# Kernel tuning notes

Measured on AMD Instinct MI355X. Metric: run time of the kernel, lower is better.

## Reference

```python
import jax, jax.numpy as jnp
import numpy as np

DIM = 512
N_HEADS = 8
HEAD_DIM = DIM // N_HEADS
BN_EPS = 1e-5


def setup_inputs() -> dict:
    key = jax.random.key(0)
    ks = jax.random.split(key, 8)
    B, C, H, W = 16, DIM, 32, 32
    x = jax.random.normal(ks[0], (B, C, H, W), dtype=jnp.float32)
    # 1x1 convs == channel matmuls: stacked q/k/v weights [3, out, in], proj [out, in]
    w_qkv = jax.random.normal(ks[1], (3, DIM, DIM), dtype=jnp.float32) * (DIM ** -0.5)
    w_proj = jax.random.normal(ks[2], (DIM, DIM), dtype=jnp.float32) * (DIM ** -0.5)
    # BatchNorm (inference form) params for q/k/v branches, stacked [3, C]
    bn_gamma = jax.random.uniform(ks[3], (3, DIM), minval=0.5, maxval=1.5)
    bn_beta = jax.random.normal(ks[4], (3, DIM)) * 0.1
    bn_mean = jax.random.normal(ks[5], (3, DIM)) * 0.1
    bn_var = jax.random.uniform(ks[6], (3, DIM), minval=0.5, maxval=1.5)
    return {"x": x, "w_qkv": w_qkv, "w_proj": w_proj, "bn_gamma": bn_gamma,
            "bn_beta": bn_beta, "bn_mean": bn_mean, "bn_var": bn_var}


def _ternary_ste(t):
    # forward: sign(t) in {-1,0,1}; backward: identity (straight-through)
    return t + jax.lax.stop_gradient(jnp.sign(t) - t)


def reference(x, w_qkv, w_proj, bn_gamma, bn_beta, bn_mean, bn_var):
    B, C, H, W = x.shape
    N = H * W
    xf = x.reshape(B, C, N)
    # fused 1x1 conv for q,k,v: [3,B,C,N]
    qkv = jnp.einsum('koc,bcn->kbon', w_qkv, xf)
    # BatchNorm (inference): y = (x - mean)/sqrt(var+eps)*gamma + beta
    s = bn_gamma / jnp.sqrt(bn_var + BN_EPS)          # [3,C]
    b = bn_beta - bn_mean * s                          # [3,C]
    qkv = qkv * s[:, None, :, None] + b[:, None, :, None]
    q = _ternary_ste(qkv[0]).reshape(B, N_HEADS, HEAD_DIM, N)
    k = _ternary_ste(qkv[1]).reshape(B, N_HEADS, HEAD_DIM, N)
    v = qkv[2].reshape(B, N_HEADS, HEAD_DIM, N)
    scale = HEAD_DIM ** -0.5
    attn = jnp.einsum('bhdn,bhen->bhde', q, k) * scale  # [B,h,d,d] channel-wise attn
    attn = jax.nn.softmax(attn, axis=-1)
    out = jnp.einsum('bhde,bhen->bhdn', attn, v).reshape(B, C, N)
    out = jnp.einsum('oc,bcn->bon', w_proj, out) + xf   # proj + residual
    return out.reshape(B, C, H, W)
```

## Files before the change

kernel.cpp:

```cpp
#include <hip/hip_runtime.h>
#include <math.h>

#define BN_EPS 1e-5f
#define FIXC 1.0e-4f

typedef _Float16 f16;
typedef _Float16 f16x4 __attribute__((ext_vector_type(4)));
typedef _Float16 f16x8 __attribute__((ext_vector_type(8)));
typedef float f32x4 __attribute__((ext_vector_type(4)));
typedef int i32x4 __attribute__((ext_vector_type(4)));

static constexpr int BB = 16;
static constexpr int C  = 512;
static constexpr int NP = 1024;
static constexpr int NH = 8;
static constexpr int HD = 64;
static constexpr int M3 = 1536;


static constexpr size_t OFF_WHI  = 0;
static constexpr size_t OFF_WLO  = 1572864;
static constexpr size_t OFF_WPH  = 3145728;
static constexpr size_t OFF_SB   = 3670016;
static constexpr size_t OFF_WN   = 3682304;
static constexpr size_t OFF_XN   = 3686400;
static constexpr size_t OFF_FLAG = 3751936;
static constexpr size_t OFF_XTH  = 5849088;
static constexpr size_t OFF_XTL  = 22626304;
static constexpr size_t OFF_AOT  = OFF_XTH;
static constexpr size_t OFF_Q    = 39403520;
static constexpr size_t OFF_K    = 47792128;
static constexpr size_t OFF_VT   = 56180736;

__device__ __forceinline__ void gld16(const void* g, void* l) {
  __builtin_amdgcn_global_load_lds(
      (const __attribute__((address_space(1))) void*)g,
      (__attribute__((address_space(3))) void*)l, 16, 0, 0);
}

__device__ __forceinline__ size_t frag_off(int tile, int kt, int row7, int k5) {
  return (((size_t)tile * 16 + kt) * 8 + (row7 >> 4)) * 512
       + (size_t)((row7 & 15) | ((k5 >> 3) << 4)) * 8;
}

__global__ __launch_bounds__(256) void k_convW(
    const float* __restrict__ wqkv, const float* __restrict__ wproj,
    const float* __restrict__ g, const float* __restrict__ be,
    const float* __restrict__ mu, const float* __restrict__ va,
    f16* __restrict__ Whi, f16* __restrict__ Wlo, f16* __restrict__ Wph,
    float* __restrict__ sA, float* __restrict__ bA, float* __restrict__ wnorm)
{
  const int i = blockIdx.x * 256 + threadIdx.x;
  {
    const int m = i >> 6, l = i & 63;
    const float4 v0 = *(const float4*)&wqkv[(size_t)m * C + l * 8];
    const float4 v1 = *(const float4*)&wqkv[(size_t)m * C + l * 8 + 4];
    const float vv[8] = {v0.x, v0.y, v0.z, v0.w, v1.x, v1.y, v1.z, v1.w};
    f16x8 hv, lv;
    float s2 = 0.f;
#pragma unroll
    for (int q = 0; q < 8; ++q) {
      const f16 h = (f16)vv[q];
      hv[q] = h; lv[q] = (f16)(vv[q] - (float)h);
      s2 = fmaf(vv[q], vv[q], s2);
    }
    *(f16x8*)&Whi[frag_off(m >> 7, l >> 2, m & 127, (l & 3) * 8)] = hv;
    *(f16x8*)&Wlo[(size_t)m * C + l * 8] = lv;
    if (m < 1024) {
      s2 += __shfl_xor(s2, 1);  s2 += __shfl_xor(s2, 2);
      s2 += __shfl_xor(s2, 4);  s2 += __shfl_xor(s2, 8);
      s2 += __shfl_xor(s2, 16); s2 += __shfl_xor(s2, 32);
      if (l == 0) wnorm[m] = sqrtf(s2);
    }
  }
  if (i < 32768) {
    const int m = i >> 6, l = i & 63;
    const float4 v0 = *(const float4*)&wproj[(size_t)m * C + l * 8];
    const float4 v1 = *(const float4*)&wproj[(size_t)m * C + l * 8 + 4];
    const float vv[8] = {v0.x, v0.y, v0.z, v0.w, v1.x, v1.y, v1.z, v1.w};
    f16x8 hv;
#pragma unroll
    for (int q = 0; q < 8; ++q) hv[q] = (f16)vv[q];
    *(f16x8*)&Wph[frag_off(m >> 7, l >> 2, m & 127, (l & 3) * 8)] = hv;
  }
  if (i < M3) {
    const float s = g[i] / sqrtf(va[i] + BN_EPS);
    sA[i] = s;
    bA[i] = be[i] - mu[i] * s;
  }
}

__global__ __launch_bounds__(256) void k_convX(
    const float* __restrict__ x, f16* __restrict__ XtH, f16* __restrict__ XtL,
    float* __restrict__ xnorm2)
{
  const int k0 = blockIdx.x * 64, n0 = blockIdx.y * 64, b = blockIdx.z;
  __shared__ float ls[64][65];
  const int t = threadIdx.x;
  const float* xp = x + ((size_t)b * C + k0) * NP + n0;
  const int c4 = (t & 15) * 4, r0 = t >> 4;
#pragma unroll
  for (int q = 0; q < 4; ++q) {
    const float4 v = *(const float4*)(xp + (size_t)(r0 + q * 16) * NP + c4);
    ls[r0 + q * 16][c4 + 0] = v.x; ls[r0 + q * 16][c4 + 1] = v.y;
    ls[r0 + q * 16][c4 + 2] = v.z; ls[r0 + q * 16][c4 + 3] = v.w;
  }
  __syncthreads();
  if (t < 64) {
    float s2 = 0.f;
#pragma unroll
    for (int q = 0; q < 64; ++q) { const float v = ls[q][t]; s2 = fmaf(v, v, s2); }
    atomicAdd(&xnorm2[(b << 10) + n0 + t], s2);
  }
  const int n = t >> 2, kk = (t & 3) * 16;
  const int n_abs = n0 + n;
  f16x8 hv0 = {}, hv1 = {}, lv0 = {}, lv1 = {};
#pragma unroll
  for (int q = 0; q < 8; ++q) {
    const float v = ls[kk + q][n];
    const f16 h = (f16)v;
    hv0[q] = h; lv0[q] = (f16)(v - (float)h);
  }
#pragma unroll
  for (int q = 0; q < 8; ++q) {
    const float v = ls[kk + 8 + q][n];
    const f16 h = (f16)v;
    hv1[q] = h; lv1[q] = (f16)(v - (float)h);
  }
  const int kb0 = k0 + kk, kb1 = k0 + kk + 8;
  *(f16x8*)&XtH[frag_off(b * 8 + (n_abs >> 7), kb0 >> 5, n_abs & 127, kb0 & 31)] = hv0;
  *(f16x8*)&XtH[frag_off(b * 8 + (n_abs >> 7), kb1 >> 5, n_abs & 127, kb1 & 31)] = hv1;
  *(f16x8*)&XtL[((size_t)b * NP + n_abs) * C + kb0] = lv0;
  *(f16x8*)&XtL[((size_t)b * NP + n_abs) * C + kb1] = lv1;
}

__global__ __launch_bounds__(64, 3) void k_qkv_mfma(
    const f16* __restrict__ Whi, const f16* __restrict__ XtH,
    const float* __restrict__ sA, const float* __restrict__ bA,
    const float* __restrict__ wnorm, const float* __restrict__ xnorm2,
    signed char* __restrict__ qw, signed char* __restrict__ kw,
    f16* __restrict__ vt, unsigned* __restrict__ flagbits)
{
  __shared__ __align__(16) f16 SMEM[64 * 72];

  const int lane = threadIdx.x;
  const int n0 = blockIdx.x * 64, m0 = blockIdx.y * 64, b = blockIdx.z;

  const f16* Af = Whi + (size_t)(m0 >> 7) * 65536;
  const f16* Bf = XtH + ((size_t)b * 8 + (n0 >> 7)) * 65536;
  const int ab = (m0 >> 4) & 7;
  const int bb = (n0 >> 4) & 7;

  f32x4 acc[4][4];
#pragma unroll
  for (int i = 0; i < 4; ++i)
#pragma unroll
    for (int j = 0; j < 4; ++j) acc[i][j] = (f32x4){0.f, 0.f, 0.f, 0.f};

  const int lr = lane & 15, ls = lane >> 4;

#define LOADF(KT, AR, BR) do {                                          \
    _Pragma("unroll")                                                   \
    for (int i_ = 0; i_ < 4; ++i_) {                                    \
      (AR)[i_] = *(const f16x8*)&Af[((size_t)(KT) * 8 + ab + i_) * 512 + lane * 8]; \
      (BR)[i_] = *(const f16x8*)&Bf[((size_t)(KT) * 8 + bb + i_) * 512 + lane * 8]; \
    }                                                                   \
  } while (0)

#define COMPF(AR, BR) do {                                              \
    _Pragma("unroll")                                                   \
    for (int i_ = 0; i_ < 4; ++i_)                                      \
      _Pragma("unroll")                                                 \
      for (int j_ = 0; j_ < 4; ++j_)                                    \
        acc[i_][j_] = __builtin_amdgcn_mfma_f32_16x16x32_f16(           \
            (AR)[i_], (BR)[j_], acc[i_][j_], 0, 0, 0);                  \
  } while (0)

  {
    f16x8 a0[4], b0[4], a1[4], b1[4];
    LOADF(0, a0, b0);
#pragma unroll
    for (int kt = 0; kt < 16; kt += 2) {
      LOADF(kt + 1, a1, b1);
      COMPF(a0, b0);
      if (kt + 2 < 16) LOADF(kt + 2, a0, b0);
      COMPF(a1, b1);
    }
  }

#undef LOADF
#undef COMPF

  const int kidx = m0 >> 9;
  if (kidx != 2) {
    signed char* dst0 = (kidx == 0) ? qw : kw;
    float xnrm[4];
#pragma unroll
    for (int j = 0; j < 4; ++j)
      xnrm[j] = sqrtf(xnorm2[(b << 10) + n0 + j * 16 + lr]);
#pragma unroll
    for (int i = 0; i < 4; ++i) {
      float sv[4], bv[4], dl[4];
#pragma unroll
      for (int r = 0; r < 4; ++r) {
        const int o = m0 + i * 16 + ls * 4 + r;
        sv[r] = sA[o]; bv[r] = bA[o];
        dl[r] = FIXC * wnorm[o] * sv[r];
      }
      const int oc0 = (m0 & 511) + i * 16 + ls * 4;
      const int og0 = m0 + i * 16 + ls * 4;
#pragma unroll
      for (int j = 0; j < 4; ++j) {
        const int n = n0 + j * 16 + lr;
#pragma unroll
        for (int r = 0; r < 4; ++r) {
          const float z = fmaf(acc[i][j][r], sv[r], bv[r]);
          dst0[((size_t)b * C + oc0 + r) * NP + n] =
              (signed char)((z > 0.f) - (z < 0.f));
          if (fabsf(z) <= dl[r] * xnrm[j]) {
            const int of = og0 + r;
            atomicOr(&flagbits[(((size_t)b * NP + n) << 5) + (of >> 5)],
                     1u << (of & 31));
          }
        }
      }
    }
  } else {
    const int c0 = m0 & 511;
#pragma unroll
    for (int i = 0; i < 4; ++i) {
      float sv[4], bv[4];
#pragma unroll
      for (int r = 0; r < 4; ++r) {
        const int o = m0 + i * 16 + ls * 4 + r;
        sv[r] = sA[o]; bv[r] = bA[o];
      }
#pragma unroll
      for (int j = 0; j < 4; ++j) {
        f16x4 pk;
#pragma unroll
        for (int r = 0; r < 4; ++r)
          pk[r] = (f16)fmaf(acc[i][j][r], sv[r], bv[r]);
        *(f16x4*)&SMEM[(size_t)(j * 16 + lr) * 72 + i * 16 + ls * 4] = pk;
      }
    }
    __syncthreads();
    f16* dstv = vt + ((size_t)b * NP + n0 + lane) * C + c0;
#pragma unroll
    for (int q = 0; q < 8; ++q) {
      const f16x8 rq = *(const f16x8*)&SMEM[(size_t)lane * 72 + q * 8];
      *(f16x8*)(dstv + q * 8) = rq;
    }
  }
}

__global__ __launch_bounds__(256) void k_fix(
    const unsigned* __restrict__ flagbits,
    const f16* __restrict__ Whi, const f16* __restrict__ Wlo,
    const f16* __restrict__ XtH, const f16* __restrict__ XtL,
    const float* __restrict__ sA, const float* __restrict__ bA,
    signed char* __restrict__ qw, signed char* __restrict__ kw)
{
  const int wv = blockIdx.x * 4 + (threadIdx.x >> 6);
  const int lane = threadIdx.x & 63;
  const int b = wv >> 10, n = wv & 1023;

  const unsigned* bm = flagbits + ((size_t)wv << 5);
  const unsigned myw = (lane < 32) ? bm[lane] : 0u;
  if (__ballot(myw != 0) == 0ULL) return;

  const int kb = lane * 8;
  const f16x8 bhv = *(const f16x8*)&XtH[
      frag_off(b * 8 + (n >> 7), kb >> 5, n & 127, kb & 31)];
  const f16x8 blv = *(const f16x8*)&XtL[((size_t)b * NP + n) * C + kb];
  float xv[8];
#pragma unroll
  for (int q = 0; q < 8; ++q) xv[q] = (float)bhv[q] + (float)blv[q];

  for (int w = 0; w < 32; ++w) {
    unsigned bits = __shfl(myw, w);
    while (bits) {
      const int o = w * 32 + __builtin_ctz(bits);
      bits &= bits - 1;
      const f16x8 ahv = *(const f16x8*)&Whi[
          frag_off(o >> 7, kb >> 5, o & 127, kb & 31)];
      const f16x8 alv = *(const f16x8*)&Wlo[(size_t)o * C + kb];
      float s = 0.f;
#pragma unroll
      for (int q = 0; q < 8; ++q)
        s = fmaf((float)ahv[q] + (float)alv[q], xv[q], s);
      s += __shfl_xor(s, 1);  s += __shfl_xor(s, 2);  s += __shfl_xor(s, 4);
      s += __shfl_xor(s, 8);  s += __shfl_xor(s, 16); s += __shfl_xor(s, 32);
      if (lane == 0) {
        const float y = fmaf(s, sA[o], bA[o]);
        const signed char sg = (signed char)((y > 0.f) - (y < 0.f));
        if (o < 512) qw[((size_t)b * C + o) * NP + n] = sg;
        else         kw[((size_t)b * C + (o - 512)) * NP + n] = sg;
      }
    }
  }
}

__global__ __launch_bounds__(256) void k_attn_fused(
    const signed char* __restrict__ qw, const signed char* __restrict__ kw,
    const f16* __restrict__ vt, f16* __restrict__ aot)
{
  const int half = blockIdx.x;
  const int bh = blockIdx.y;
  const int b = bh >> 3, h = bh & 7;
  const int t = threadIdx.x, lane = t & 63, wid = t >> 6;
  const int dw = wid * 16;
  const int lr = lane & 15, lg = lane >> 4;

  __shared__ f16 ph[64][72];
  __shared__ f16 pl[64][72];
  __shared__ f16 sb[64][72];

  const signed char* qp = qw + ((size_t)b * C + h * HD + dw + lr) * NP;
  const signed char* kp = kw + ((size_t)b * C + h * HD + lr) * NP;

  i32x4 accS[4];
#pragma unroll
  for (int j = 0; j < 4; ++j) accS[j] = (i32x4){0, 0, 0, 0};

#pragma unroll 4
  for (int ks = 0; ks < 16; ++ks) {
    const i32x4 af = *(const i32x4*)(qp + ks * 64 + lg * 16);
#pragma unroll
    for (int j = 0; j < 4; ++j) {
      const i32x4 bf = *(const i32x4*)(kp + (size_t)(j * 16) * NP + ks * 64 + lg * 16);
      accS[j] = __builtin_amdgcn_mfma_i32_16x16x64_i8(af, bf, accS[j], 0, 0, 0);
    }
  }

#pragma unroll
  for (int r = 0; r < 4; ++r) {
    float mx = (float)accS[0][r];
#pragma unroll
    for (int j = 1; j < 4; ++j) mx = fmaxf(mx, (float)accS[j][r]);
    mx = fmaxf(mx, __shfl_xor(mx, 1));
    mx = fmaxf(mx, __shfl_xor(mx, 2));
    mx = fmaxf(mx, __shfl_xor(mx, 4));
    mx = fmaxf(mx, __shfl_xor(mx, 8));
    float pvv[4];
    float sm = 0.f;
#pragma unroll
    for (int j = 0; j < 4; ++j) {
      pvv[j] = expf(((float)accS[j][r] - mx) * 0.125f);
      sm += pvv[j];
    }
    sm += __shfl_xor(sm, 1);
    sm += __shfl_xor(sm, 2);
    sm += __shfl_xor(sm, 4);
    sm += __shfl_xor(sm, 8);
    const float inv = 1.f / sm;
    const int drow = dw + lg * 4 + r;
#pragma unroll
    for (int j = 0; j < 4; ++j) {
      const float p = pvv[j] * inv;
      const f16 hi = (f16)p;
      ph[drow][j * 16 + lr] = hi;
      pl[drow][j * 16 + lr] = (f16)(p - (float)hi);
    }
  }
  __syncthreads();

  const f16x8 pa0h = *(const f16x8*)&ph[dw + lr][lg * 8];
  const f16x8 pa0l = *(const f16x8*)&pl[dw + lr][lg * 8];
  const f16x8 pa1h = *(const f16x8*)&ph[dw + lr][32 + lg * 8];
  const f16x8 pa1l = *(const f16x8*)&pl[dw + lr][32 + lg * 8];

  const f16* vbase = vt + (size_t)b * NP * C + h * HD;
  const int nbase = half * 512;

  for (int nc = 0; nc < 8; ++nc) {
    const int nn0 = nbase + nc * 64;
    __syncthreads();
#pragma unroll
    for (int nt = 0; nt < 4; ++nt) {
      const f16* vp = vbase + (size_t)(nn0 + nt * 16 + lr) * C + lg * 8;
      const f16x8 bv0 = *(const f16x8*)(vp);
      const f16x8 bv1 = *(const f16x8*)(vp + 32);
      f32x4 acc = (f32x4){0.f, 0.f, 0.f, 0.f};
      acc = __builtin_amdgcn_mfma_f32_16x16x32_f16(pa0h, bv0, acc, 0, 0, 0);
      acc = __builtin_amdgcn_mfma_f32_16x16x32_f16(pa0l, bv0, acc, 0, 0, 0);
      acc = __builtin_amdgcn_mfma_f32_16x16x32_f16(pa1h, bv1, acc, 0, 0, 0);
      acc = __builtin_amdgcn_mfma_f32_16x16x32_f16(pa1l, bv1, acc, 0, 0, 0);
      f16x4 pk;
#pragma unroll
      for (int r = 0; r < 4; ++r) pk[r] = (f16)acc[r];
      *(f16x4*)&sb[nt * 16 + lr][dw + lg * 4] = pk;
    }
    __syncthreads();
    const int nl = t >> 2, cc = (t & 3) * 16;
    const f16x8 o0 = *(const f16x8*)&sb[nl][cc];
    const f16x8 o1 = *(const f16x8*)&sb[nl][cc + 8];
    const int n_abs = nn0 + nl;
    const int c1 = h * HD + cc, c2 = h * HD + cc + 8;
    *(f16x8*)&aot[frag_off(b * 8 + (n_abs >> 7), c1 >> 5, n_abs & 127, c1 & 31)] = o0;
    *(f16x8*)&aot[frag_off(b * 8 + (n_abs >> 7), c2 >> 5, n_abs & 127, c2 & 31)] = o1;
  }
}

__global__ __launch_bounds__(256) void k_proj_mfma(
    const f16* __restrict__ Wph, const f16* __restrict__ aot,
    const float* __restrict__ X, float* __restrict__ out)
{
  __shared__ __align__(16) f16 SMEM[32768];
  f16* const As0 = SMEM;
  f16* const Bs0 = SMEM + 8192;
  f16* const As1 = SMEM + 16384;
  f16* const Bs1 = SMEM + 24576;

  const int t = threadIdx.x, lane = t & 63, wid = t >> 6;
  const int n0 = blockIdx.x * 128, m0 = blockIdx.y * 128, b = blockIdx.z;

  const f16* Af = Wph + (size_t)(m0 >> 7) * 65536;
  const f16* Bf = aot + ((size_t)b * 8 + (n0 >> 7)) * 65536;

  f32x4 acc[4][4];
#pragma unroll
  for (int i = 0; i < 4; ++i)
#pragma unroll
    for (int j = 0; j < 4; ++j) acc[i][j] = (f32x4){0.f, 0.f, 0.f, 0.f};

  const int wm = wid >> 1, wn = wid & 1;
  const int lr = lane & 15, ls = lane >> 4;
  const int soff = wid * 512 + lane * 8;

#define PSTAGE(TI, AS, BS) do {                                         \
    const f16* Ak_ = Af + (size_t)(TI) * 8192;                          \
    const f16* Bk_ = Bf + (size_t)(TI) * 8192;                          \
    _Pragma("unroll")                                                   \
    for (int r_ = 0; r_ < 4; ++r_) {                                    \
      gld16(Ak_ + r_ * 2048 + soff, &(AS)[r_ * 2048 + wid * 512]);      \
      gld16(Bk_ + r_ * 2048 + soff, &(BS)[r_ * 2048 + wid * 512]);      \
    }                                                                   \
  } while (0)

#define PCOMP(AS, BS) do {                                              \
    _Pragma("unroll")                                                   \
    for (int ksub_ = 0; ksub_ < 2; ++ksub_) {                           \
      f16x8 ah_[4], bh_[4];                                             \
      _Pragma("unroll")                                                 \
      for (int i_ = 0; i_ < 4; ++i_) {                                  \
        ah_[i_] = *(const f16x8*)&(AS)[ksub_ * 4096 + (wm * 4 + i_) * 512 + lane * 8]; \
        bh_[i_] = *(const f16x8*)&(BS)[ksub_ * 4096 + (wn * 4 + i_) * 512 + lane * 8]; \
      }                                                                 \
      _Pragma("unroll")                                                 \
      for (int i_ = 0; i_ < 4; ++i_)                                    \
        _Pragma("unroll")                                               \
        for (int j_ = 0; j_ < 4; ++j_)                                  \
          acc[i_][j_] = __builtin_amdgcn_mfma_f32_16x16x32_f16(         \
              ah_[i_], bh_[j_], acc[i_][j_], 0, 0, 0);                  \
    }                                                                   \
  } while (0)

  PSTAGE(0, As0, Bs0);
#pragma unroll
  for (int ti = 0; ti < 8; ++ti) {
    if (ti < 7) {
      if (ti & 1) PSTAGE(ti + 1, As0, Bs0);
      else        PSTAGE(ti + 1, As1, Bs1);
      asm volatile("s_waitcnt vmcnt(8)" ::: "memory");
    } else {
      asm volatile("s_waitcnt vmcnt(0)" ::: "memory");
    }
    __builtin_amdgcn_sched_barrier(0);
    __builtin_amdgcn_s_barrier();
    if (ti & 1) PCOMP(As1, Bs1); else PCOMP(As0, Bs0);
    asm volatile("s_waitcnt lgkmcnt(0)" ::: "memory");
    __builtin_amdgcn_sched_barrier(0);
    __builtin_amdgcn_s_barrier();
  }

#undef PSTAGE
#undef PCOMP

#pragma unroll
  for (int i = 0; i < 4; ++i) {
    const int oc0 = m0 + wm * 64 + i * 16 + ls * 4;
#pragma unroll
    for (int j = 0; j < 4; ++j) {
      const int n = n0 + wn * 64 + j * 16 + lr;
#pragma unroll
      for (int r = 0; r < 4; ++r) {
        const size_t idx = ((size_t)b * C + oc0 + r) * NP + n;
        out[idx] = acc[i][j][r] + X[idx];
      }
    }
  }
}

extern "C" void kernel_launch(void* const* d_in, const int* in_sizes, int n_in,
                              void* d_out, int out_size, void* d_ws, size_t ws_size,
                              hipStream_t stream)
{
  const float* x      = (const float*)d_in[0];
  const float* w_qkv  = (const float*)d_in[1];
  const float* w_proj = (const float*)d_in[2];
  const float* g      = (const float*)d_in[3];
  const float* be     = (const float*)d_in[4];
  const float* mu     = (const float*)d_in[5];
  const float* va     = (const float*)d_in[6];
  float* out = (float*)d_out;

  char* ws = (char*)d_ws;
  f16*  Whi = (f16*)(ws + OFF_WHI);
  f16*  Wlo = (f16*)(ws + OFF_WLO);
  f16*  Wph = (f16*)(ws + OFF_WPH);
  float* sA = (float*)(ws + OFF_SB);
  float* bA = sA + M3;
  float* wn = (float*)(ws + OFF_WN);
  float* xn2 = (float*)(ws + OFF_XN);
  unsigned* flagbits = (unsigned*)(ws + OFF_FLAG);
  f16*  XtH = (f16*)(ws + OFF_XTH);
  f16*  XtL = (f16*)(ws + OFF_XTL);
  f16*  aot = (f16*)(ws + OFF_AOT);
  signed char* qw = (signed char*)(ws + OFF_Q);
  signed char* kw = (signed char*)(ws + OFF_K);
  f16*  vtw = (f16*)(ws + OFF_VT);

  hipMemsetAsync(xn2, 0, OFF_XTH - OFF_XN, stream);

  k_convW<<<dim3(384), 256, 0, stream>>>(
      w_qkv, w_proj, g, be, mu, va, Whi, Wlo, Wph, sA, bA, wn);
  k_convX<<<dim3(C / 64, NP / 64, BB), 256, 0, stream>>>(x, XtH, XtL, xn2);
  k_qkv_mfma<<<dim3(NP / 64, M3 / 64, BB), 64, 0, stream>>>(
      Whi, XtH, sA, bA, wn, xn2, qw, kw, vtw, flagbits);
  k_fix<<<dim3(BB * NP / 4), 256, 0, stream>>>(
      flagbits, Whi, Wlo, XtH, XtL, sA, bA, qw, kw);
  k_attn_fused<<<dim3(2, BB * NH), 256, 0, stream>>>(qw, kw, vtw, aot);
  k_proj_mfma<<<dim3(NP / 128, C / 128, BB), 256, 0, stream>>>(Wph, aot, x, out);
}
```

Baseline: 145.8 us.

## Retile QKV GEMM to 256x256 block tiles with double-buffered LDS staging

```diff
diff --git a/kernel.cpp b/kernel.cpp
--- a/kernel.cpp
+++ b/kernel.cpp
@@ -134,62 +134,82 @@
   *(f16x8*)&XtL[((size_t)b * NP + n_abs) * C + kb1] = lv1;
 }
 
-__global__ __launch_bounds__(64, 3) void k_qkv_mfma(
+__global__ __launch_bounds__(512, 1) void k_qkv_mfma(
     const f16* __restrict__ Whi, const f16* __restrict__ XtH,
     const float* __restrict__ sA, const float* __restrict__ bA,
     const float* __restrict__ wnorm, const float* __restrict__ xnorm2,
     signed char* __restrict__ qw, signed char* __restrict__ kw,
     f16* __restrict__ vt, unsigned* __restrict__ flagbits)
 {
-  __shared__ __align__(16) f16 SMEM[64 * 72];
-
-  const int lane = threadIdx.x;
-  const int n0 = blockIdx.x * 64, m0 = blockIdx.y * 64, b = blockIdx.z;
+  __shared__ __align__(16) f16 SMEM[65536];
+  f16* const As0 = SMEM;
+  f16* const Bs0 = SMEM + 16384;
+  f16* const As1 = SMEM + 32768;
+  f16* const Bs1 = SMEM + 49152;
+
+  const int t = threadIdx.x, lane = t & 63, wid = t >> 6;
+  const int n0 = blockIdx.x * 256, m0 = blockIdx.y * 256, b = blockIdx.z;
 
   const f16* Af = Whi + (size_t)(m0 >> 7) * 65536;
   const f16* Bf = XtH + ((size_t)b * 8 + (n0 >> 7)) * 65536;
-  const int ab = (m0 >> 4) & 7;
-  const int bb = (n0 >> 4) & 7;
-
-  f32x4 acc[4][4];
-#pragma unroll
-  for (int i = 0; i < 4; ++i)
+
+  f32x4 acc[8][4];
+#pragma unroll
+  for (int i = 0; i < 8; ++i)
 #pragma unroll
     for (int j = 0; j < 4; ++j) acc[i][j] = (f32x4){0.f, 0.f, 0.f, 0.f};
 
+  const int wm = wid >> 2, wn = wid & 3;
   const int lr = lane & 15, ls = lane >> 4;
 
-#define LOADF(KT, AR, BR) do {                                          \
+#define QSTAGE(S, AS, BS) do {                                          \
     _Pragma("unroll")                                                   \
-    for (int i_ = 0; i_ < 4; ++i_) {                                    \
-      (AR)[i_] = *(const f16x8*)&Af[((size_t)(KT) * 8 + ab + i_) * 512 + lane * 8]; \
-      (BR)[i_] = *(const f16x8*)&Bf[((size_t)(KT) * 8 + bb + i_) * 512 + lane * 8]; \
+    for (int u_ = 0; u_ < 4; ++u_) {                                    \
+      const size_t so_ = (size_t)(u_ >> 1) * 65536 +                    \
+                         (size_t)(2 * (S) + (u_ & 1)) * 4096 + t * 8;   \
+      gld16(Af + so_, &(AS)[u_ * 4096 + wid * 512]);                    \
+      gld16(Bf + so_, &(BS)[u_ * 4096 + wid * 512]);                    \
     }                                                                   \
   } while (0)
 
-#define COMPF(AR, BR) do {                                              \
-    _Pragma("unroll")                                                   \
-    for (int i_ = 0; i_ < 4; ++i_)                                      \
-      _Pragma("unroll")                                                 \
-      for (int j_ = 0; j_ < 4; ++j_)                                    \
-        acc[i_][j_] = __builtin_amdgcn_mfma_f32_16x16x32_f16(           \
-            (AR)[i_], (BR)[j_], acc[i_][j_], 0, 0, 0);                  \
-  } while (0)
-
-  {
-    f16x8 a0[4], b0[4], a1[4], b1[4];
-    LOADF(0, a0, b0);
-#pragma unroll
-    for (int kt = 0; kt < 16; kt += 2) {
-      LOADF(kt + 1, a1, b1);
-      COMPF(a0, b0);
-      if (kt + 2 < 16) LOADF(kt + 2, a0, b0);
-      COMPF(a1, b1);
-    }
-  }
-
-#undef LOADF
-#undef COMPF
+  QSTAGE(0, As0, Bs0);
+#pragma unroll
+  for (int s = 0; s < 8; ++s) {
+    if (s < 7) {
+      if (s & 1) QSTAGE(s + 1, As0, Bs0);
+      else       QSTAGE(s + 1, As1, Bs1);
+      asm volatile("s_waitcnt vmcnt(8)" ::: "memory");
+    } else {
+      asm volatile("s_waitcnt vmcnt(0)" ::: "memory");
+    }
+    __builtin_amdgcn_sched_barrier(0);
+    __builtin_amdgcn_s_barrier();
+    const f16* AS = (s & 1) ? As1 : As0;
+    const f16* BS = (s & 1) ? Bs1 : Bs0;
+#pragma unroll
+    for (int ph = 0; ph < 4; ++ph) {
+      const int mh = ph & 1, ksub = ph >> 1;
+      f16x8 ah[4], bh[4];
+#pragma unroll
+      for (int ii = 0; ii < 4; ++ii)
+        ah[ii] = *(const f16x8*)&AS[((wm * 2 + ksub) * 8 + mh * 4 + ii) * 512 + lane * 8];
+#pragma unroll
+      for (int j = 0; j < 4; ++j)
+        bh[j] = *(const f16x8*)&BS[(((wn >> 1) * 2 + ksub) * 8 + (wn & 1) * 4 + j) * 512 + lane * 8];
+      __builtin_amdgcn_s_setprio(1);
+#pragma unroll
+      for (int ii = 0; ii < 4; ++ii)
+#pragma unroll
+        for (int j = 0; j < 4; ++j)
+          acc[mh * 4 + ii][j] = __builtin_amdgcn_mfma_f32_16x16x32_f16(
+              ah[ii], bh[j], acc[mh * 4 + ii][j], 0, 0, 0);
+      __builtin_amdgcn_s_setprio(0);
+    }
+    asm volatile("s_waitcnt lgkmcnt(0)" ::: "memory");
+    __builtin_amdgcn_sched_barrier(0);
+    __builtin_amdgcn_s_barrier();
+  }
+#undef QSTAGE
 
   const int kidx = m0 >> 9;
   if (kidx != 2) {
@@ -197,21 +217,21 @@
     float xnrm[4];
 #pragma unroll
     for (int j = 0; j < 4; ++j)
-      xnrm[j] = sqrtf(xnorm2[(b << 10) + n0 + j * 16 + lr]);
-#pragma unroll
-    for (int i = 0; i < 4; ++i) {
+      xnrm[j] = sqrtf(xnorm2[(b << 10) + n0 + wn * 64 + j * 16 + lr]);
+#pragma unroll
+    for (int i = 0; i < 8; ++i) {
       float sv[4], bv[4], dl[4];
 #pragma unroll
       for (int r = 0; r < 4; ++r) {
-        const int o = m0 + i * 16 + ls * 4 + r;
+        const int o = m0 + wm * 128 + i * 16 + ls * 4 + r;
         sv[r] = sA[o]; bv[r] = bA[o];
         dl[r] = FIXC * wnorm[o] * sv[r];
       }
-      const int oc0 = (m0 & 511) + i * 16 + ls * 4;
-      const int og0 = m0 + i * 16 + ls * 4;
+      const int oc0 = (m0 & 511) + wm * 128 + i * 16 + ls * 4;
+      const int og0 = m0 + wm * 128 + i * 16 + ls * 4;
 #pragma unroll
       for (int j = 0; j < 4; ++j) {
-        const int n = n0 + j * 16 + lr;
+        const int n = n0 + wn * 64 + j * 16 + lr;
 #pragma unroll
         for (int r = 0; r < 4; ++r) {
           const float z = fmaf(acc[i][j][r], sv[r], bv[r]);
@@ -227,29 +247,35 @@
     }
   } else {
     const int c0 = m0 & 511;
-#pragma unroll
-    for (int i = 0; i < 4; ++i) {
-      float sv[4], bv[4];
-#pragma unroll
-      for (int r = 0; r < 4; ++r) {
-        const int o = m0 + i * 16 + ls * 4 + r;
-        sv[r] = sA[o]; bv[r] = bA[o];
+    for (int hc = 0; hc < 2; ++hc) {
+      __syncthreads();
+      if (wm == hc) {
+#pragma unroll
+        for (int i = 0; i < 8; ++i) {
+          float sv[4], bv[4];
+#pragma unroll
+          for (int r = 0; r < 4; ++r) {
+            const int o = m0 + wm * 128 + i * 16 + ls * 4 + r;
+            sv[r] = sA[o]; bv[r] = bA[o];
+          }
+#pragma unroll
+          for (int j = 0; j < 4; ++j) {
+            const int n_local = wn * 64 + j * 16 + lr;
+            f16x4 pk;
+#pragma unroll
+            for (int r = 0; r < 4; ++r)
+              pk[r] = (f16)fmaf(acc[i][j][r], sv[r], bv[r]);
+            *(f16x4*)&SMEM[(size_t)n_local * 136 + i * 16 + ls * 4] = pk;
+          }
+        }
       }
-#pragma unroll
-      for (int j = 0; j < 4; ++j) {
-        f16x4 pk;
-#pragma unroll
-        for (int r = 0; r < 4; ++r)
-          pk[r] = (f16)fmaf(acc[i][j][r], sv[r], bv[r]);
-        *(f16x4*)&SMEM[(size_t)(j * 16 + lr) * 72 + i * 16 + ls * 4] = pk;
-      }
-    }
-    __syncthreads();
-    f16* dstv = vt + ((size_t)b * NP + n0 + lane) * C + c0;
-#pragma unroll
-    for (int q = 0; q < 8; ++q) {
-      const f16x8 rq = *(const f16x8*)&SMEM[(size_t)lane * 72 + q * 8];
-      *(f16x8*)(dstv + q * 8) = rq;
+      __syncthreads();
+      const int n_l = t >> 1, coff = (t & 1) * 64;
+      f16* dstv = vt + ((size_t)b * NP + n0 + n_l) * C + c0 + hc * 128 + coff;
+      const f16* src = &SMEM[(size_t)n_l * 136 + coff];
+#pragma unroll
+      for (int q = 0; q < 8; ++q)
+        *(f16x8*)(dstv + q * 8) = *(const f16x8*)(src + q * 8);
     }
   }
 }
@@ -526,7 +552,7 @@
   k_convW<<<dim3(384), 256, 0, stream>>>(
       w_qkv, w_proj, g, be, mu, va, Whi, Wlo, Wph, sA, bA, wn);
   k_convX<<<dim3(C / 64, NP / 64, BB), 256, 0, stream>>>(x, XtH, XtL, xn2);
-  k_qkv_mfma<<<dim3(NP / 64, M3 / 64, BB), 64, 0, stream>>>(
+  k_qkv_mfma<<<dim3(NP / 256, M3 / 256, BB), 512, 0, stream>>>(
       Whi, XtH, sA, bA, wn, xn2, qw, kw, vtw, flagbits);
   k_fix<<<dim3(BB * NP / 4), 256, 0, stream>>>(
       flagbits, Whi, Wlo, XtH, XtL, sA, bA, qw, kw);
```

Result: faster. 142.4 us (-2.3%).
